# Optimization experiments

Measured on AMD Instinct MI355X. Metric: run time of the kernel, lower is better.

Reference implementation:

```python
import jax, jax.numpy as jnp
import numpy as np

B, N, C, K = 4, 4096, 512, 20
HID = C // 8  # dim // downrate
EPS = 1e-5
SLOPE = 0.2


def leaky_relu(x):
    return jnp.where(x >= 0, x, SLOPE * x)


def setup_inputs() -> dict:
    key = jax.random.key(0)
    k1, k2, k3, k4 = jax.random.split(key, 4)
    x_features = jax.random.normal(k1, (B, N, C), dtype=jnp.float32)
    xyz_coords = jax.random.normal(k2, (B, N, 3), dtype=jnp.float32)
    # conv1: Conv2d(2C -> HID, 1x1, bias=False) as dense matrix (HID, 2C)
    w1 = jax.random.normal(k3, (HID, 2 * C), dtype=jnp.float32) * (1.0 / np.sqrt(2 * C))
    g1 = jnp.ones((HID,), jnp.float32)
    b1 = jnp.zeros((HID,), jnp.float32)
    # conv2: Conv1d(HID -> C, 1, bias=False) as (C, HID)
    w2 = jax.random.normal(k4, (C, HID), dtype=jnp.float32) * (1.0 / np.sqrt(HID))
    g2 = jnp.ones((C,), jnp.float32)
    b2 = jnp.zeros((C,), jnp.float32)
    return {"x_features": x_features, "xyz_coords": xyz_coords,
            "w1": w1, "g1": g1, "b1": b1, "w2": w2, "g2": g2, "b2": b2}


def _knn_idx(xyz):
    # pairwise squared distance: ||a||^2 + ||b||^2 - 2 a.b  -> (B, N, N)
    sq = jnp.sum(xyz * xyz, -1)
    d = sq[:, :, None] + sq[:, None, :] - 2.0 * jnp.einsum('bnc,bmc->bnm', xyz, xyz)
    # topk smallest == topk largest of -d
    _, idx = jax.lax.top_k(-d, K)  # (B, N, K)
    return idx


def reference(x_features, xyz_coords, w1, g1, b1, w2, g2, b2):
    idx = _knn_idx(xyz_coords)  # (B,N,K) int32
    # gather neighbor features: (B,N,K,C)
    neigh = x_features[jnp.arange(B)[:, None, None], idx]
    query = x_features[:, :, None, :]  # (B,N,1,C)
    # fused = [neigh - query, query] along channels -> (B,N,K,2C)
    fused = jnp.concatenate([neigh - query, jnp.broadcast_to(query, neigh.shape)], axis=-1)
    # conv1 (1x1) -> (B,N,K,HID)
    h = jnp.einsum('bnkc,dc->bnkd', fused, w1)
    # BatchNorm2d over (B,N,K) per channel (training-mode batch stats, biased var)
    mu = jnp.mean(h, axis=(0, 1, 2))
    var = jnp.mean((h - mu) ** 2, axis=(0, 1, 2))
    h = leaky_relu(g1 * (h - mu) * jax.lax.rsqrt(var + EPS) + b1)
    # max over k neighbors -> (B,N,HID)
    h = jnp.max(h, axis=2)
    # conv2 (1x1) -> (B,N,C)
    y = jnp.einsum('bnd,ed->bne', h, w2)
    mu2 = jnp.mean(y, axis=(0, 1))
    var2 = jnp.mean((y - mu2) ** 2, axis=(0, 1))
    y = leaky_relu(g2 * (y - mu2) * jax.lax.rsqrt(var2 + EPS) + b2)
    return y  # (B, N, C), matches output_features.permute(0,2,1)
```

## Files before the change

### kernel.cpp

```cpp
#include <hip/hip_runtime.h>
#include <hip/hip_bf16.h>
#include <stdint.h>

#define NPTS 4096
#define NBATCH 4
#define NCH 512
#define NK 20
#define NHID 64
#define NROWS 16384
#define S1SH 32
#define S2SH 16

typedef __attribute__((ext_vector_type(8))) short bf16x8;
typedef __attribute__((ext_vector_type(4))) float f32x4;

__device__ __forceinline__ float bf2f(unsigned short u) {
    return __uint_as_float(((unsigned)u) << 16);
}
__device__ __forceinline__ unsigned short f2bf(float f) {
    unsigned u = __float_as_uint(f);
    unsigned r = 0x7FFFu + ((u >> 16) & 1u);
    return (unsigned short)((u + r) >> 16);
}
__device__ __forceinline__ float leaky(float x) { return x >= 0.f ? x : 0.2f * x; }
__device__ __forceinline__ int dtflag(const void* g) {
    return (((const unsigned short*)g)[0] == 0x3F80u) ? 0 : 1;
}

__device__ __forceinline__ void split8(const float* p, bf16x8& hi, bf16x8& lo) {
    float4 v0 = *(const float4*)p;
    float4 v1 = *(const float4*)(p + 4);
    float vv[8] = {v0.x, v0.y, v0.z, v0.w, v1.x, v1.y, v1.z, v1.w};
#pragma unroll
    for (int i = 0; i < 8; ++i) {
        unsigned u = __float_as_uint(vv[i]);
        hi[i] = (short)(u >> 16);
        float hf = __uint_as_float(u & 0xFFFF0000u);
        lo[i] = (short)f2bf(vv[i] - hf);
    }
}

template <int CTRL, int RM>
__device__ __forceinline__ float dppmin_f(float v) {
    int s = __builtin_amdgcn_update_dpp(__float_as_int(v), __float_as_int(v), CTRL, RM, 0xF, false);
    return fminf(v, __int_as_float(s));
}
template <int CTRL, int RM>
__device__ __forceinline__ unsigned dppmin_u(unsigned v) {
    unsigned s = (unsigned)__builtin_amdgcn_update_dpp((int)v, (int)v, CTRL, RM, 0xF, false);
    return v < s ? v : s;
}
__device__ __forceinline__ float wave_min_f63(float v) {
    v = dppmin_f<0x111, 0xF>(v);
    v = dppmin_f<0x112, 0xF>(v);
    v = dppmin_f<0x114, 0xF>(v);
    v = dppmin_f<0x118, 0xF>(v);
    v = dppmin_f<0x142, 0xA>(v);
    v = dppmin_f<0x143, 0xC>(v);
    return v;
}
__device__ __forceinline__ unsigned wave_min_u63(unsigned v) {
    v = dppmin_u<0x111, 0xF>(v);
    v = dppmin_u<0x112, 0xF>(v);
    v = dppmin_u<0x114, 0xF>(v);
    v = dppmin_u<0x118, 0xF>(v);
    v = dppmin_u<0x142, 0xA>(v);
    v = dppmin_u<0x143, 0xC>(v);
    return v;
}

__global__ __launch_bounds__(256) void k_wsplit(const float* __restrict__ w1f,
                                                const float* __restrict__ w2f,
                                                const void* __restrict__ g1,
                                                unsigned short* __restrict__ Whi,
                                                unsigned short* __restrict__ Wlo,
                                                unsigned short* __restrict__ Wh2,
                                                unsigned short* __restrict__ Wl2,
                                                float* __restrict__ sumsz) {
    int t = threadIdx.x;
    int id = blockIdx.x * 256 + t;
    sumsz[id] = 0.f;
    if (id < 20480 - 16384) sumsz[id + 16384] = 0.f;
    if (dtflag(g1) != 1) return;
    {
        int e0 = id * 4;
        int n = e0 >> 9, k = e0 & 511;
        const float* src = w1f + ((n < 64) ? (size_t)n * 1024 + k
                                           : (size_t)(n - 64) * 1024 + 512 + k);
        float4 v = *(const float4*)src;
        float vv[4] = {v.x, v.y, v.z, v.w};
        unsigned short hs[4], ls[4];
#pragma unroll
        for (int i = 0; i < 4; ++i) {
            unsigned u = __float_as_uint(vv[i]);
            hs[i] = (unsigned short)(u >> 16);
            float hf = __uint_as_float(u & 0xFFFF0000u);
            ls[i] = f2bf(vv[i] - hf);
        }
        *(ushort4*)(Whi + e0) = make_ushort4(hs[0], hs[1], hs[2], hs[3]);
        *(ushort4*)(Wlo + e0) = make_ushort4(ls[0], ls[1], ls[2], ls[3]);
    }
    {
        int e0 = id * 2;
        float2 v = *(const float2*)(w2f + e0);
        float vv[2] = {v.x, v.y};
        unsigned short hs[2], ls[2];
#pragma unroll
        for (int i = 0; i < 2; ++i) {
            unsigned u = __float_as_uint(vv[i]);
            hs[i] = (unsigned short)(u >> 16);
            float hf = __uint_as_float(u & 0xFFFF0000u);
            ls[i] = f2bf(vv[i] - hf);
        }
        *(ushort2*)(Wh2 + e0) = make_ushort2(hs[0], hs[1]);
        *(ushort2*)(Wl2 + e0) = make_ushort2(ls[0], ls[1]);
    }
}

__global__ __launch_bounds__(256) void k_pq(const void* __restrict__ xv,
                                            const unsigned short* __restrict__ w1u,
                                            const unsigned short* __restrict__ Whi,
                                            const unsigned short* __restrict__ Wlo,
                                            float* __restrict__ PQ,
                                            const void* __restrict__ g1) {
    int f = dtflag(g1);
    int t = threadIdx.x;
    int l = t & 63, w = t >> 6;
    int m0 = blockIdx.x * 16;
    int lr = l & 15, lk = (l >> 4) * 8;
    int n0a = w * 32, n0b = n0a + 16;
    f32x4 acc0 = {0.f, 0.f, 0.f, 0.f};
    f32x4 acc1 = {0.f, 0.f, 0.f, 0.f};
    if (!f) {
        const unsigned short* xp = (const unsigned short*)xv + (size_t)(m0 + lr) * 512 + lk;
        int na = n0a + lr, nb = n0b + lr;
        size_t wao = (na < 64) ? (size_t)na * 1024 : (size_t)(na - 64) * 1024 + 512;
        size_t wbo = (nb < 64) ? (size_t)nb * 1024 : (size_t)(nb - 64) * 1024 + 512;
        const unsigned short* wpa = w1u + wao + lk;
        const unsigned short* wpb = w1u + wbo + lk;
#pragma unroll 4
        for (int k0 = 0; k0 < 512; k0 += 32) {
            bf16x8 a  = *(const bf16x8*)(xp + k0);
            bf16x8 b0 = *(const bf16x8*)(wpa + k0);
            bf16x8 b1 = *(const bf16x8*)(wpb + k0);
            acc0 = __builtin_amdgcn_mfma_f32_16x16x32_bf16(a, b0, acc0, 0, 0, 0);
            acc1 = __builtin_amdgcn_mfma_f32_16x16x32_bf16(a, b1, acc1, 0, 0, 0);
        }
    } else {
        const float* xp = (const float*)xv + (size_t)(m0 + lr) * 512 + lk;
        const unsigned short* wha = Whi + (size_t)(n0a + lr) * 512 + lk;
        const unsigned short* wla = Wlo + (size_t)(n0a + lr) * 512 + lk;
        const unsigned short* whb = Whi + (size_t)(n0b + lr) * 512 + lk;
        const unsigned short* wlb = Wlo + (size_t)(n0b + lr) * 512 + lk;
        f32x4 hh0 = {0.f,0.f,0.f,0.f}, hl0 = {0.f,0.f,0.f,0.f}, lh0 = {0.f,0.f,0.f,0.f};
        f32x4 hh1 = {0.f,0.f,0.f,0.f}, hl1 = {0.f,0.f,0.f,0.f}, lh1 = {0.f,0.f,0.f,0.f};
#pragma unroll 4
        for (int k0 = 0; k0 < 512; k0 += 32) {
            bf16x8 ah, al;
            split8(xp + k0, ah, al);
            bf16x8 bh0 = *(const bf16x8*)(wha + k0);
            bf16x8 bl0 = *(const bf16x8*)(wla + k0);
            bf16x8 bh1 = *(const bf16x8*)(whb + k0);
            bf16x8 bl1 = *(const bf16x8*)(wlb + k0);
            hh0 = __builtin_amdgcn_mfma_f32_16x16x32_bf16(ah, bh0, hh0, 0, 0, 0);
            hh1 = __builtin_amdgcn_mfma_f32_16x16x32_bf16(ah, bh1, hh1, 0, 0, 0);
            hl0 = __builtin_amdgcn_mfma_f32_16x16x32_bf16(ah, bl0, hl0, 0, 0, 0);
            hl1 = __builtin_amdgcn_mfma_f32_16x16x32_bf16(ah, bl1, hl1, 0, 0, 0);
            lh0 = __builtin_amdgcn_mfma_f32_16x16x32_bf16(al, bh0, lh0, 0, 0, 0);
            lh1 = __builtin_amdgcn_mfma_f32_16x16x32_bf16(al, bh1, lh1, 0, 0, 0);
        }
#pragma unroll
        for (int r = 0; r < 4; ++r) {
            acc0[r] = hh0[r] + hl0[r] + lh0[r];
            acc1[r] = hh1[r] + hl1[r] + lh1[r];
        }
    }
    int cr = (l >> 4) * 4, cc = l & 15;
    float* o = PQ + (size_t)(m0 + cr) * 128;
#pragma unroll
    for (int r = 0; r < 4; ++r) {
        o[(size_t)r * 128 + n0a + cc] = acc0[r];
        o[(size_t)r * 128 + n0b + cc] = acc1[r];
    }
}

__global__ __launch_bounds__(512) void k_knn(const void* __restrict__ xyzv,
                                             int* __restrict__ idxb,
                                             const void* __restrict__ g1) {
    __shared__ float spx[NPTS], spy[NPTS], spz[NPTS];
    const float FINF = __int_as_float(0x7F800000);
    int f = dtflag(g1);
    int t = threadIdx.x;
    int b = blockIdx.y;
    for (int p = t; p < NPTS; p += 512) {
        size_t base = ((size_t)b * NPTS + p) * 3;
        float fx, fy, fz;
        if (!f) {
            const unsigned short* xu = (const unsigned short*)xyzv;
            fx = bf2f(xu[base]); fy = bf2f(xu[base + 1]); fz = bf2f(xu[base + 2]);
        } else {
            const float* xf = (const float*)xyzv;
            fx = xf[base]; fy = xf[base + 1]; fz = xf[base + 2];
        }
        spx[p] = fx; spy[p] = fy; spz[p] = fz;
    }
    __syncthreads();
    int lane = t & 63, wave = t >> 6;
    int nl = blockIdx.x * 8 + wave;
    float qx = spx[nl], qy = spy[nl], qz = spz[nl];
    float sqn = __fadd_rn(__fadd_rn(__fmul_rn(qx, qx), __fmul_rn(qy, qy)), __fmul_rn(qz, qz));
    float D[64];
    float gv[8]; int gj[8];
#pragma unroll
    for (int g = 0; g < 8; ++g) { gv[g] = FINF; gj[g] = 0; }
#pragma unroll
    for (int j = 0; j < 64; ++j) {
        float px = spx[j * 64 + lane], py = spy[j * 64 + lane], pz = spz[j * 64 + lane];
        float psq = __fadd_rn(__fadd_rn(__fmul_rn(px, px), __fmul_rn(py, py)), __fmul_rn(pz, pz));
        float dot = __fadd_rn(__fadd_rn(__fmul_rn(qx, px), __fmul_rn(qy, py)),
                              __fmul_rn(qz, pz));
        float d = __fsub_rn(__fadd_rn(sqn, psq), __fmul_rn(2.0f, dot));
        D[j] = d;
        int g = j >> 3;
        bool lt = d < gv[g];
        gv[g] = lt ? d : gv[g];
        gj[g] = lt ? j : gj[g];
    }
    int myout = 0;
    for (int k = 0; k < NK; ++k) {
        float bv = gv[0]; int bj = gj[0];
#pragma unroll
        for (int g = 1; g < 8; ++g) {
            bool lt = gv[g] < bv;
            bv = lt ? gv[g] : bv;
            bj = lt ? gj[g] : bj;
        }
        float red = wave_min_f63(bv);
        float s_mv = __int_as_float(__builtin_amdgcn_readlane(__float_as_int(red), 63));
        unsigned long long tied = __ballot(bv == s_mv);
        int sL, sj;
        if (__popcll(tied) == 1) {
            sL = (int)__builtin_ctzll(tied);
            sj = __builtin_amdgcn_readlane(bj, sL);
        } else {
            unsigned bjm = (bv == s_mv) ? (unsigned)bj : 0xFFFFFFFFu;
            unsigned rj = wave_min_u63(bjm);
            sj = __builtin_amdgcn_readlane((int)rj, 63);
            unsigned long long t2 = __ballot((bv == s_mv) && (bj == sj));
            sL = (int)__builtin_ctzll(t2);
        }
        int sm = (sj << 6) | sL;
        if (lane == k) myout = sm;
        bool iwin = (lane == sL);
#pragma unroll
        for (int gg = 0; gg < 8; ++gg) {
            if (gg == (sj >> 3)) {
#pragma unroll
                for (int jj = 0; jj < 8; ++jj) {
                    int j = gg * 8 + jj;
                    bool rem = iwin && (j == sj);
                    D[j] = rem ? FINF : D[j];
                }
                float nv = D[gg * 8]; int nj = gg * 8;
#pragma unroll
                for (int u = 1; u < 8; ++u) {
                    bool lt = D[gg * 8 + u] < nv;
                    nv = lt ? D[gg * 8 + u] : nv;
                    nj = lt ? gg * 8 + u : nj;
                }
                if (iwin) { gv[gg] = nv; gj[gg] = nj; }
            }
        }
    }
    if (lane < NK)
        idxb[((size_t)b * NPTS + nl) * NK + lane] = myout;
}

__global__ __launch_bounds__(256) void k_gather(const float* __restrict__ PQ,
                                                const int* __restrict__ idxb,
                                                float* __restrict__ Hmax,
                                                float* __restrict__ Hmin,
                                                float* __restrict__ sums1) {
    __shared__ float bs[64], bq[64];
    int t = threadIdx.x;
    if (t < 64) { bs[t] = 0.f; bq[t] = 0.f; }
    __syncthreads();
    int lane = t & 63, wave = t >> 6;
    int rowbase = blockIdx.x * 16 + wave * 4;
    int b = blockIdx.x >> 8;
    size_t boff = (size_t)b * NPTS;
    float lsum = 0.f, lsq = 0.f;
    for (int r = 0; r < 4; ++r) {
        int row = rowbase + r;
        float q = PQ[(size_t)row * 128 + 64 + lane] - PQ[(size_t)row * 128 + lane];
        const int* ip = idxb + (size_t)row * NK;
        int idx[20];
        *(int4*)&idx[0]  = *(const int4*)(ip + 0);
        *(int4*)&idx[4]  = *(const int4*)(ip + 4);
        *(int4*)&idx[8]  = *(const int4*)(ip + 8);
        *(int4*)&idx[12] = *(const int4*)(ip + 12);
        *(int4*)&idx[16] = *(const int4*)(ip + 16);
        float hmax = -3.4e38f, hmin = 3.4e38f;
#pragma unroll
        for (int k = 0; k < NK; ++k) {
            int m = idx[k] & (NPTS - 1);
            float p = PQ[(boff + m) * 128 + lane];
            float h = p + q;
            lsum += h; lsq += h * h;
            hmax = fmaxf(hmax, h); hmin = fminf(hmin, h);
        }
        Hmax[(size_t)row * 64 + lane] = hmax;
        Hmin[(size_t)row * 64 + lane] = hmin;
    }
    atomicAdd(&bs[lane], lsum);
    atomicAdd(&bq[lane], lsq);
    __syncthreads();
    float* sh = sums1 + (blockIdx.x & (S1SH - 1)) * 128;
    if (t < 64) { atomicAdd(&sh[t], bs[t]); atomicAdd(&sh[64 + t], bq[t]); }
}

__global__ __launch_bounds__(256) void k_gemm2(const float* __restrict__ Hmax,
                                               const float* __restrict__ Hmin,
                                               const float* __restrict__ sums1,
                                               const void* __restrict__ g1,
                                               const void* __restrict__ b1,
                                               const unsigned short* __restrict__ Wh2,
                                               const unsigned short* __restrict__ Wl2,
                                               const void* __restrict__ w2raw,
                                               void* __restrict__ out,
                                               float* __restrict__ sums2) {
    int f = dtflag(g1);
    __shared__ float a1s[64], c1s[64];
    __shared__ float s2[512], q2[512];
    int t = threadIdx.x;
    s2[t] = 0.f; s2[t + 256] = 0.f; q2[t] = 0.f; q2[t + 256] = 0.f;
    if (t < 64) {
        float ssum = 0.f, ssq = 0.f;
#pragma unroll 4
        for (int s = 0; s < S1SH; ++s) {
            ssum += sums1[s * 128 + t];
            ssq  += sums1[s * 128 + 64 + t];
        }
        const float inv = 1.0f / 327680.0f;
        float mu = ssum * inv;
        float var = fmaxf(ssq * inv - mu * mu, 0.f);
        float rstd = rsqrtf(var + 1e-5f);
        float gvv = f ? ((const float*)g1)[t] : bf2f(((const unsigned short*)g1)[t]);
        float bvv = f ? ((const float*)b1)[t] : bf2f(((const unsigned short*)b1)[t]);
        float a = gvv * rstd;
        a1s[t] = a;
        c1s[t] = bvv - mu * a;
    }
    __syncthreads();
    int lane = t & 63, w = t >> 6;
    int lr = lane & 15, lk = (lane >> 4) * 8;
    int rowo = blockIdx.x * 16;
    int row = rowo + lr;
    bf16x8 ah[2], al[2];
#pragma unroll
    for (int c = 0; c < 2; ++c) {
        int off = c * 32 + lk;
        const float* Mx = Hmax + (size_t)row * 64 + off;
        const float* Mn = Hmin + (size_t)row * 64 + off;
        float4 M0 = *(const float4*)Mx, M1 = *(const float4*)(Mx + 4);
        float4 m0 = *(const float4*)Mn, m1 = *(const float4*)(Mn + 4);
        float Ms[8] = {M0.x, M0.y, M0.z, M0.w, M1.x, M1.y, M1.z, M1.w};
        float ms[8] = {m0.x, m0.y, m0.z, m0.w, m1.x, m1.y, m1.z, m1.w};
#pragma unroll
        for (int e = 0; e < 8; ++e) {
            float A = a1s[off + e], C = c1s[off + e];
            float h = leaky(A * (A >= 0.f ? Ms[e] : ms[e]) + C);
            unsigned u = __float_as_uint(h);
            ah[c][e] = (short)(u >> 16);
            al[c][e] = (short)f2bf(h - __uint_as_float(u & 0xFFFF0000u));
        }
    }
    int cr = (lane >> 4) * 4, cc = lane & 15;
#pragma unroll 2
    for (int j = 0; j < 8; ++j) {
        int n0 = w * 128 + j * 16;
        f32x4 hh = {0.f,0.f,0.f,0.f}, hl = {0.f,0.f,0.f,0.f}, lh = {0.f,0.f,0.f,0.f};
        if (!f) {
            const unsigned short* wb = (const unsigned short*)w2raw + (size_t)(n0 + lr) * 64;
            bf16x8 b0 = *(const bf16x8*)(wb + lk);
            bf16x8 b1 = *(const bf16x8*)(wb + 32 + lk);
            hh = __builtin_amdgcn_mfma_f32_16x16x32_bf16(ah[0], b0, hh, 0, 0, 0);
            lh = __builtin_amdgcn_mfma_f32_16x16x32_bf16(al[0], b0, lh, 0, 0, 0);
            hh = __builtin_amdgcn_mfma_f32_16x16x32_bf16(ah[1], b1, hh, 0, 0, 0);
            lh = __builtin_amdgcn_mfma_f32_16x16x32_bf16(al[1], b1, lh, 0, 0, 0);
        } else {
            const unsigned short* bh = Wh2 + (size_t)(n0 + lr) * 64;
            const unsigned short* bl = Wl2 + (size_t)(n0 + lr) * 64;
            bf16x8 bh0 = *(const bf16x8*)(bh + lk), bl0 = *(const bf16x8*)(bl + lk);
            bf16x8 bh1 = *(const bf16x8*)(bh + 32 + lk), bl1 = *(const bf16x8*)(bl + 32 + lk);
            hh = __builtin_amdgcn_mfma_f32_16x16x32_bf16(ah[0], bh0, hh, 0, 0, 0);
            hl = __builtin_amdgcn_mfma_f32_16x16x32_bf16(ah[0], bl0, hl, 0, 0, 0);
            lh = __builtin_amdgcn_mfma_f32_16x16x32_bf16(al[0], bh0, lh, 0, 0, 0);
            hh = __builtin_amdgcn_mfma_f32_16x16x32_bf16(ah[1], bh1, hh, 0, 0, 0);
            hl = __builtin_amdgcn_mfma_f32_16x16x32_bf16(ah[1], bl1, hl, 0, 0, 0);
            lh = __builtin_amdgcn_mfma_f32_16x16x32_bf16(al[1], bh1, lh, 0, 0, 0);
        }
        float se = 0.f, sqe = 0.f;
#pragma unroll
        for (int r = 0; r < 4; ++r) {
            float y = hh[r] + hl[r] + lh[r];
            se += y; sqe += y * y;
            size_t oi = (size_t)(rowo + cr + r) * 512 + n0 + cc;
            if (!f) ((unsigned short*)out)[oi] = f2bf(y);
            else    ((float*)out)[oi] = y;
        }
        se += __shfl_xor(se, 16, 64);  se += __shfl_xor(se, 32, 64);
        sqe += __shfl_xor(sqe, 16, 64); sqe += __shfl_xor(sqe, 32, 64);
        if ((lane >> 4) == 0) {
            atomicAdd(&s2[n0 + cc], se);
            atomicAdd(&q2[n0 + cc], sqe);
        }
    }
    __syncthreads();
    float* s2g = sums2 + (blockIdx.x & (S2SH - 1)) * 1024;
    atomicAdd(&s2g[t], s2[t]);
    atomicAdd(&s2g[t + 256], s2[t + 256]);
    atomicAdd(&s2g[512 + t], q2[t]);
    atomicAdd(&s2g[512 + t + 256], q2[t + 256]);
}

__global__ void k_stats2(const float* __restrict__ sums2,
                         const void* __restrict__ g2,
                         const void* __restrict__ b2,
                         float* __restrict__ a2c2) {
    int f = dtflag(g2);
    int t = threadIdx.x;
    float ssum = 0.f, ssq = 0.f;
#pragma unroll
    for (int s = 0; s < S2SH; ++s) {
        ssum += sums2[s * 1024 + t];
        ssq  += sums2[s * 1024 + 512 + t];
    }
    const float inv = 1.0f / 16384.0f;
    float mu = ssum * inv;
    float var = fmaxf(ssq * inv - mu * mu, 0.f);
    float rstd = rsqrtf(var + 1e-5f);
    float gvv = f ? ((const float*)g2)[t] : bf2f(((const unsigned short*)g2)[t]);
    float bvv = f ? ((const float*)b2)[t] : bf2f(((const unsigned short*)b2)[t]);
    float a = gvv * rstd;
    a2c2[t] = a;
    a2c2[512 + t] = bvv - mu * a;
}

__global__ __launch_bounds__(256) void k_final(void* __restrict__ out,
                                               const float* __restrict__ a2c2,
                                               const void* __restrict__ g2) {
    int f = dtflag(g2);
    size_t base = ((size_t)blockIdx.x * 256 + threadIdx.x) * 8;
    int e0 = (int)(base & 511);
    float a[8], c[8];
    *(float4*)&a[0] = *(const float4*)&a2c2[e0];
    *(float4*)&a[4] = *(const float4*)&a2c2[e0 + 4];
    *(float4*)&c[0] = *(const float4*)&a2c2[512 + e0];
    *(float4*)&c[4] = *(const float4*)&a2c2[512 + e0 + 4];
    if (!f) {
        unsigned short* po = (unsigned short*)out + base;
        uint4 v = *(const uint4*)po;
        unsigned w[4] = {v.x, v.y, v.z, v.w};
        unsigned r[4];
#pragma unroll
        for (int i = 0; i < 4; ++i) {
            float f0 = __uint_as_float(w[i] << 16);
            float f1 = __uint_as_float(w[i] & 0xFFFF0000u);
            float y0 = leaky(a[2 * i] * f0 + c[2 * i]);
            float y1 = leaky(a[2 * i + 1] * f1 + c[2 * i + 1]);
            r[i] = (unsigned)f2bf(y0) | ((unsigned)f2bf(y1) << 16);
        }
        *(uint4*)po = make_uint4(r[0], r[1], r[2], r[3]);
    } else {
        float* po = (float*)out + base;
        float4 v0 = *(const float4*)po;
        float4 v1 = *(const float4*)(po + 4);
        float v[8] = {v0.x, v0.y, v0.z, v0.w, v1.x, v1.y, v1.z, v1.w};
#pragma unroll
        for (int i = 0; i < 8; ++i) v[i] = leaky(a[i] * v[i] + c[i]);
        *(float4*)po = make_float4(v[0], v[1], v[2], v[3]);
        *(float4*)(po + 4) = make_float4(v[4], v[5], v[6], v[7]);
    }
}

extern "C" void kernel_launch(void* const* d_in, const int* in_sizes, int n_in,
                              void* d_out, int out_size, void* d_ws, size_t ws_size,
                              hipStream_t stream) {
    const void* x   = d_in[0];
    const void* xyz = d_in[1];
    const void* w1  = d_in[2];
    const void* g1  = d_in[3];
    const void* b1  = d_in[4];
    const void* w2  = d_in[5];
    const void* g2  = d_in[6];
    const void* b2  = d_in[7];

    float* ws    = (float*)d_ws;
    float* PQ    = ws;
    float* Hmax  = ws + 2097152;
    float* Hmin  = ws + 3145728;
    float* sums1 = ws + 4194304;
    float* sums2 = ws + 4198400;
    float* a2c2  = ws + 4214784;
    int*   idxb  = (int*)(ws + 4215808);
    unsigned short* Whi = (unsigned short*)(ws + 4543488);
    unsigned short* Wlo = (unsigned short*)(ws + 4576256);
    unsigned short* Wh2 = (unsigned short*)(ws + 4609024);
    unsigned short* Wl2 = (unsigned short*)(ws + 4625408);

    k_wsplit<<<64, 256, 0, stream>>>((const float*)w1, (const float*)w2, g1,
                                     Whi, Wlo, Wh2, Wl2, sums1);
    k_pq<<<1024, 256, 0, stream>>>(x, (const unsigned short*)w1, Whi, Wlo, PQ, g1);
    k_knn<<<dim3(512, 4), 512, 0, stream>>>(xyz, idxb, g1);
    k_gather<<<1024, 256, 0, stream>>>(PQ, idxb, Hmax, Hmin, sums1);
    k_gemm2<<<1024, 256, 0, stream>>>(Hmax, Hmin, sums1, g1, b1,
                                      Wh2, Wl2, w2, d_out, sums2);
    k_stats2<<<1, 512, 0, stream>>>(sums2, g2, b2, a2c2);
    k_final<<<4096, 256, 0, stream>>>(d_out, a2c2, g2);
}
```

Before: 251.7 us.

## Stage split x tile in LDS and reorder W1 hi/lo into k-blocked layout

In the fp32 path of k_pq, each block now splits its 16x512 x tile into bf16 hi/lo once and stores it in shared memory. Previously each of the four waves re-split the same rows from global memory. The hi/lo W1 copies are rewritten in a k-blocked layout (k/8, n, 8) so the B-fragment loads of a wave are contiguous across lanes. This cuts redundant conversion work and improves load coalescing, at the cost of about 33KB of LDS and a block barrier.

```diff
diff --git a/kernel.cpp b/kernel.cpp
--- a/kernel.cpp
+++ b/kernel.cpp
@@ -25,19 +25,6 @@
 __device__ __forceinline__ float leaky(float x) { return x >= 0.f ? x : 0.2f * x; }
 __device__ __forceinline__ int dtflag(const void* g) {
     return (((const unsigned short*)g)[0] == 0x3F80u) ? 0 : 1;
-}
-
-__device__ __forceinline__ void split8(const float* p, bf16x8& hi, bf16x8& lo) {
-    float4 v0 = *(const float4*)p;
-    float4 v1 = *(const float4*)(p + 4);
-    float vv[8] = {v0.x, v0.y, v0.z, v0.w, v1.x, v1.y, v1.z, v1.w};
-#pragma unroll
-    for (int i = 0; i < 8; ++i) {
-        unsigned u = __float_as_uint(vv[i]);
-        hi[i] = (short)(u >> 16);
-        float hf = __uint_as_float(u & 0xFFFF0000u);
-        lo[i] = (short)f2bf(vv[i] - hf);
-    }
 }
 
 template <int CTRL, int RM>
@@ -97,8 +84,9 @@
             float hf = __uint_as_float(u & 0xFFFF0000u);
             ls[i] = f2bf(vv[i] - hf);
         }
-        *(ushort4*)(Whi + e0) = make_ushort4(hs[0], hs[1], hs[2], hs[3]);
-        *(ushort4*)(Wlo + e0) = make_ushort4(ls[0], ls[1], ls[2], ls[3]);
+        size_t dst = ((size_t)(k >> 3) * 128 + n) * 8 + (k & 7);
+        *(ushort4*)(Whi + dst) = make_ushort4(hs[0], hs[1], hs[2], hs[3]);
+        *(ushort4*)(Wlo + dst) = make_ushort4(ls[0], ls[1], ls[2], ls[3]);
     }
     {
         int e0 = id * 2;
@@ -123,11 +111,12 @@
                                             const unsigned short* __restrict__ Wlo,
                                             float* __restrict__ PQ,
                                             const void* __restrict__ g1) {
+    __shared__ unsigned short xh[16][520], xl[16][520];
     int f = dtflag(g1);
     int t = threadIdx.x;
     int l = t & 63, w = t >> 6;
     int m0 = blockIdx.x * 16;
-    int lr = l & 15, lk = (l >> 4) * 8;
+    int lr = l & 15, q = l >> 4, lk = q * 8;
     int n0a = w * 32, n0b = n0a + 16;
     f32x4 acc0 = {0.f, 0.f, 0.f, 0.f};
     f32x4 acc1 = {0.f, 0.f, 0.f, 0.f};
@@ -147,21 +136,40 @@
             acc1 = __builtin_amdgcn_mfma_f32_16x16x32_bf16(a, b1, acc1, 0, 0, 0);
         }
     } else {
-        const float* xp = (const float*)xv + (size_t)(m0 + lr) * 512 + lk;
-        const unsigned short* wha = Whi + (size_t)(n0a + lr) * 512 + lk;
-        const unsigned short* wla = Wlo + (size_t)(n0a + lr) * 512 + lk;
-        const unsigned short* whb = Whi + (size_t)(n0b + lr) * 512 + lk;
-        const unsigned short* wlb = Wlo + (size_t)(n0b + lr) * 512 + lk;
+        const float* xf = (const float*)xv + (size_t)m0 * 512;
+#pragma unroll
+        for (int j = 0; j < 8; ++j) {
+            int e = j * 1024 + t * 4;
+            int row = e >> 9, col = e & 511;
+            float4 v = *(const float4*)(xf + e);
+            float vv[4] = {v.x, v.y, v.z, v.w};
+            unsigned short hs[4], ls[4];
+#pragma unroll
+            for (int i = 0; i < 4; ++i) {
+                unsigned u = __float_as_uint(vv[i]);
+                hs[i] = (unsigned short)(u >> 16);
+                float hf = __uint_as_float(u & 0xFFFF0000u);
+                ls[i] = f2bf(vv[i] - hf);
+            }
+            *(ushort4*)&xh[row][col] = make_ushort4(hs[0], hs[1], hs[2], hs[3]);
+            *(ushort4*)&xl[row][col] = make_ushort4(ls[0], ls[1], ls[2], ls[3]);
+        }
+        __syncthreads();
+        const unsigned short* wha = Whi + ((size_t)q * 128 + n0a + lr) * 8;
+        const unsigned short* wla = Wlo + ((size_t)q * 128 + n0a + lr) * 8;
+        const unsigned short* whb = Whi + ((size_t)q * 128 + n0b + lr) * 8;
+        const unsigned short* wlb = Wlo + ((size_t)q * 128 + n0b + lr) * 8;
         f32x4 hh0 = {0.f,0.f,0.f,0.f}, hl0 = {0.f,0.f,0.f,0.f}, lh0 = {0.f,0.f,0.f,0.f};
         f32x4 hh1 = {0.f,0.f,0.f,0.f}, hl1 = {0.f,0.f,0.f,0.f}, lh1 = {0.f,0.f,0.f,0.f};
 #pragma unroll 4
         for (int k0 = 0; k0 < 512; k0 += 32) {
-            bf16x8 ah, al;
-            split8(xp + k0, ah, al);
-            bf16x8 bh0 = *(const bf16x8*)(wha + k0);
-            bf16x8 bl0 = *(const bf16x8*)(wla + k0);
-            bf16x8 bh1 = *(const bf16x8*)(whb + k0);
-            bf16x8 bl1 = *(const bf16x8*)(wlb + k0);
+            bf16x8 ah = *(const bf16x8*)&xh[lr][k0 + lk];
+            bf16x8 al = *(const bf16x8*)&xl[lr][k0 + lk];
+            size_t wo = (size_t)k0 * 128;
+            bf16x8 bh0 = *(const bf16x8*)(wha + wo);
+            bf16x8 bl0 = *(const bf16x8*)(wla + wo);
+            bf16x8 bh1 = *(const bf16x8*)(whb + wo);
+            bf16x8 bl1 = *(const bf16x8*)(wlb + wo);
             hh0 = __builtin_amdgcn_mfma_f32_16x16x32_bf16(ah, bh0, hh0, 0, 0, 0);
             hh1 = __builtin_amdgcn_mfma_f32_16x16x32_bf16(ah, bh1, hh1, 0, 0, 0);
             hl0 = __builtin_amdgcn_mfma_f32_16x16x32_bf16(ah, bl0, hl0, 0, 0, 0);
@@ -175,7 +183,7 @@
             acc1[r] = hh1[r] + hl1[r] + lh1[r];
         }
     }
-    int cr = (l >> 4) * 4, cc = l & 15;
+    int cr = q * 4, cc = l & 15;
     float* o = PQ + (size_t)(m0 + cr) * 128;
 #pragma unroll
     for (int r = 0; r < 4; ++r) {
```

New measurement: 224.2 us. -10.9%, faster.
